# Optimization experiments

Measured on AMD Instinct MI355X. Metric: run time of the kernel, lower is better.

Reference implementation:

```python
import jax, jax.numpy as jnp
import numpy as np

B, S, H = 2, 2048, 2048
N_HEADS = 16
HEAD_DIM = H // N_HEADS  # 128


def apply_rotary(x, cos, sin):
    # x: (B, n_heads, S, head_dim); cos/sin: (S, head_dim//2)
    d = x.shape[-1] // 2
    x1, x2 = x[..., :d], x[..., d:]
    c = cos[None, None, :x.shape[2]]
    s = sin[None, None, :x.shape[2]]
    return jnp.concatenate([x1 * c - x2 * s, x2 * c + x1 * s], axis=-1)


def setup_inputs() -> dict:
    key = jax.random.key(0)
    k1, k2, k3 = jax.random.split(key, 3)
    x = jax.random.normal(k1, (B, S, H), dtype=jnp.float32)
    qkv_w = jax.random.normal(k2, (3 * H, H), dtype=jnp.float32) * (1.0 / np.sqrt(H))
    o_w = jax.random.normal(k3, (H, H), dtype=jnp.float32) * (1.0 / np.sqrt(H))
    # rotary tables, half head_dim
    inv_freq = 1.0 / (10000.0 ** (jnp.arange(0, HEAD_DIM // 2, dtype=jnp.float32) / (HEAD_DIM // 2)))
    t = jnp.arange(S, dtype=jnp.float32)
    freqs = jnp.outer(t, inv_freq)  # (S, head_dim//2)
    cos, sin = jnp.cos(freqs), jnp.sin(freqs)
    # True = masked (strictly upper triangular)
    causal_mask = jnp.triu(jnp.ones((S, S), dtype=bool), k=1)
    return {"x": x, "qkv_w": qkv_w, "o_w": o_w, "cos": cos, "sin": sin,
            "causal_mask": causal_mask}


def reference(x, qkv_w, o_w, cos, sin, causal_mask):
    Bx, Sx, Hx = x.shape
    qkv = jnp.einsum('bsh,oh->bso', x, qkv_w)  # (B,S,3H)
    qkv = qkv.reshape(Bx, Sx, 3, N_HEADS, HEAD_DIM)
    q, k, v = qkv[:, :, 0], qkv[:, :, 1], qkv[:, :, 2]
    q = jnp.transpose(q, (0, 2, 1, 3))  # (B,nh,S,hd)
    k = jnp.transpose(k, (0, 2, 1, 3))
    v = jnp.transpose(v, (0, 2, 1, 3))
    q = apply_rotary(q, cos, sin)
    k = apply_rotary(k, cos, sin)
    scale = 1.0 / jnp.sqrt(jnp.asarray(HEAD_DIM, dtype=x.dtype))
    attn = jnp.einsum('bnqd,bnkd->bnqk', q, k) * scale
    attn = jnp.where(causal_mask[None, None], -jnp.inf, attn)
    attn = jax.nn.softmax(attn, axis=-1)
    out = jnp.einsum('bnqk,bnkd->bnqd', attn, v)
    out = jnp.transpose(out, (0, 2, 1, 3)).reshape(Bx, Sx, Hx)
    return jnp.einsum('bsh,oh->bso', out, o_w)
```

## Files before the change

### kernel.cpp

```cpp
#include <hip/hip_runtime.h>
#include <hip/hip_bf16.h>
#include <stdint.h>

typedef __attribute__((ext_vector_type(4))) float f32x4;
typedef __attribute__((ext_vector_type(8))) short s16x8;
typedef __attribute__((ext_vector_type(4))) short s16x4;

#define SWZ(g, row) ((((g) & ~7) | (((g) ^ ((row) & 7)) & 7)))

__device__ __forceinline__ unsigned short f2bf(float f) {
  unsigned u = __builtin_bit_cast(unsigned, f);
  u += 0x7fffu + ((u >> 16) & 1u);
  return (unsigned short)(u >> 16);
}

__device__ __forceinline__ void gld16(const void* g, void* l) {
  __builtin_amdgcn_global_load_lds(
      (const __attribute__((address_space(1))) void*)g,
      (__attribute__((address_space(3))) void*)l, 16, 0, 0);
}

__global__ void cvt_f32_to_bf16(const float* __restrict__ src,
                                unsigned short* __restrict__ dst, int n4) {
  int i = blockIdx.x * blockDim.x + threadIdx.x;
  if (i >= n4) return;
  float4 v = ((const float4*)src)[i];
  s16x4 o;
  o[0] = (short)f2bf(v.x); o[1] = (short)f2bf(v.y);
  o[2] = (short)f2bf(v.z); o[3] = (short)f2bf(v.w);
  ((s16x4*)dst)[i] = o;
}

template<int EPI>
__global__ __launch_bounds__(256) void gemm_bt(
    const unsigned short* __restrict__ A,
    const unsigned short* __restrict__ Bt,
    float* __restrict__ C, int N, int K,
    const float* __restrict__ cosT, const float* __restrict__ sinT,
    unsigned short* __restrict__ qOut, unsigned short* __restrict__ kOut,
    unsigned short* __restrict__ vtOut)
{
  __shared__ char smem[32768];
  const int tid = (int)threadIdx.x;
  const int w  = tid >> 6, l = tid & 63;
  const int lg = l & 15, hg = l >> 4;
  const int bn0 = (int)blockIdx.x * 128, bm0 = (int)blockIdx.y * 128;

  f32x4 acc[2][8] = {};
  const int nkt = K >> 6;
  for (int kt = 0; kt < nkt; ++kt) {
    __syncthreads();
    for (int i = 0; i < 4; ++i) {
      const int G = w * 256 + i * 64 + l;
      const int row = G >> 3, g = G & 7;
      const int gs = SWZ(g, row);
      gld16((const char*)(A  + (size_t)(bm0 + row) * K + (size_t)kt * 64) + (gs << 4),
            smem + w * 4096 + i * 1024);
      gld16((const char*)(Bt + (size_t)(bn0 + row) * K + (size_t)kt * 64) + (gs << 4),
            smem + 16384 + w * 4096 + i * 1024);
    }
    asm volatile("s_waitcnt vmcnt(0)" ::: "memory");
    __syncthreads();
    for (int ks = 0; ks < 2; ++ks) {
      s16x8 af[2], bfr[8];
      for (int ai = 0; ai < 2; ++ai) {
        const int ra = w * 32 + ai * 16 + lg;
        const int gr = SWZ(4 * ks + hg, ra);
        af[ai] = *(const s16x8*)(smem + ra * 128 + (gr << 4));
      }
      for (int bi = 0; bi < 8; ++bi) {
        const int rb = bi * 16 + lg;
        const int gr = SWZ(4 * ks + hg, rb);
        bfr[bi] = *(const s16x8*)(smem + 16384 + rb * 128 + (gr << 4));
      }
      for (int ai = 0; ai < 2; ++ai)
        for (int bi = 0; bi < 8; ++bi)
          acc[ai][bi] = __builtin_amdgcn_mfma_f32_16x16x32_bf16(
              af[ai], bfr[bi], acc[ai][bi], 0, 0, 0);
    }
  }

  if constexpr (EPI == 0) {
    for (int ai = 0; ai < 2; ++ai)
      for (int bi = 0; bi < 8; ++bi) {
        const int col  = bn0 + bi * 16 + lg;
        const int row0 = bm0 + w * 32 + ai * 16 + hg * 4;
        for (int r = 0; r < 4; ++r)
          C[(size_t)(row0 + r) * N + col] = acc[ai][bi][r];
      }
  } else {
    const int t = bn0 >> 11;
    const int h = (bn0 >> 7) & 15;
    if (t < 2) {
      unsigned short* dst = (t == 0) ? qOut : kOut;
      for (int ai = 0; ai < 2; ++ai)
        for (int bi = 0; bi < 4; ++bi)
          for (int r = 0; r < 4; ++r) {
            const int gr = bm0 + w * 32 + ai * 16 + hg * 4 + r;
            const int b = gr >> 11, s1 = gr & 2047;
            const int c0 = bi * 16 + lg;
            const float x1 = acc[ai][bi][r];
            const float x2 = acc[ai][bi + 4][r];
            const float cv = cosT[s1 * 64 + c0];
            const float sv = sinT[s1 * 64 + c0];
            const size_t base = ((((size_t)b * 16 + h) * 2048) + s1) * 128;
            dst[base + c0]      = f2bf(x1 * cv - x2 * sv);
            dst[base + c0 + 64] = f2bf(x2 * cv + x1 * sv);
          }
    } else {
      for (int ai = 0; ai < 2; ++ai)
        for (int bi = 0; bi < 8; ++bi) {
          const int gr0 = bm0 + w * 32 + ai * 16 + hg * 4;
          const int b = gr0 >> 11, s0 = gr0 & 2047;
          const int d = bi * 16 + lg;
          s16x4 pk;
          for (int r = 0; r < 4; ++r) pk[r] = (short)f2bf(acc[ai][bi][r]);
          *(s16x4*)(vtOut + ((((size_t)b * 16 + h) * 128) + d) * 2048 + s0) = pk;
        }
    }
  }
}

__global__ __launch_bounds__(256) void attn_fwd(
    const unsigned short* __restrict__ Qp, const unsigned short* __restrict__ Kp,
    const unsigned short* __restrict__ Vt, unsigned short* __restrict__ AO)
{
  __shared__ char sK[16384];
  __shared__ char sV[16384];
  __shared__ char sP[8192];

  const int tid = (int)threadIdx.x, w = tid >> 6, l = tid & 63;
  const int lg = l & 15, hg = l >> 4;
  const int bid = (int)blockIdx.x;
  const int p = bid >> 8, c = bid & 255;
  const int j = c >> 5, bh = c & 31;
  const int qt = (p == 0) ? j : (p == 1) ? 31 - j : (p == 2) ? 8 + j : 23 - j;
  const size_t qkBase = (size_t)bh * 2048 * 128;
  const int qw0 = qt * 64 + w * 16;
  const int qi = qw0 + lg;

  s16x8 qf[4];
  for (int ks = 0; ks < 4; ++ks)
    qf[ks] = *(const s16x8*)(Qp + qkBase + (size_t)(qw0 + lg) * 128 + ks * 32 + hg * 8);

  f32x4 acc_o[8] = {};
  float mrun = -1e30f, lrun = 0.f;
  const float SCALE = 0.08838834764831845f;
  const float L2E = 1.4426950408889634f;
  const float CS = SCALE * L2E;

  const int nkv = qt + 1;
  for (int kv = 0; kv < nkv; ++kv) {
    const int kv0 = kv * 64;
    __syncthreads();
    for (int i = 0; i < 4; ++i) {
      const int G = w * 256 + i * 64 + l;
      const int rk = G >> 4, gk = G & 15;
      gld16((const char*)(Kp + qkBase + (size_t)(kv0 + rk) * 128) + (SWZ(gk, rk) << 4),
            sK + w * 4096 + i * 1024);
      const int rv = G >> 3, gv = G & 7;
      gld16((const char*)(Vt + qkBase + (size_t)rv * 2048 + kv0) + (SWZ(gv, rv) << 4),
            sV + w * 4096 + i * 1024);
    }
    asm volatile("s_waitcnt vmcnt(0)" ::: "memory");
    __syncthreads();

    f32x4 accs[4] = {};
    for (int ks = 0; ks < 4; ++ks)
      for (int kf = 0; kf < 4; ++kf) {
        const int row = kf * 16 + lg;
        const int g = SWZ(4 * ks + hg, row);
        s16x8 kfrag = *(const s16x8*)(sK + row * 256 + (g << 4));
        accs[kf] = __builtin_amdgcn_mfma_f32_16x16x32_bf16(kfrag, qf[ks], accs[kf], 0, 0, 0);
      }

    const bool diag = (kv == qt);
    float raw[4][4];
    float mt = -1e30f;
    #pragma unroll
    for (int kf = 0; kf < 4; ++kf)
      #pragma unroll
      for (int r = 0; r < 4; ++r) {
        float s = accs[kf][r];
        if (diag) {
          const int jj = kv0 + kf * 16 + hg * 4 + r;
          s = (jj > qi) ? -1e30f : s;
        }
        raw[kf][r] = s;
        mt = fmaxf(mt, s);
      }
    mt = fmaxf(mt, __shfl_xor(mt, 16));
    mt = fmaxf(mt, __shfl_xor(mt, 32));
    mt *= SCALE;
    if (!__all(mt - mrun <= 8.0f)) {
      const float mnew = fmaxf(mrun, mt);
      const float alpha = exp2f((mrun - mnew) * L2E);
      float ar[4];
      #pragma unroll
      for (int r = 0; r < 4; ++r) ar[r] = __shfl(alpha, hg * 4 + r);
      #pragma unroll
      for (int f = 0; f < 8; ++f)
        #pragma unroll
        for (int r = 0; r < 4; ++r) acc_o[f][r] *= ar[r];
      lrun *= alpha;
      mrun = mnew;
    }
    const float mL = mrun * L2E;
    float ls = 0.f;
    char* pw = sP + w * 2048;
    #pragma unroll
    for (int kf = 0; kf < 4; ++kf) {
      s16x4 pk;
      #pragma unroll
      for (int r = 0; r < 4; ++r) {
        const float e = exp2f(raw[kf][r] * CS - mL);
        ls += e;
        pk[r] = (short)f2bf(e);
      }
      const int j0 = kf * 16 + hg * 4;
      *(s16x4*)(pw + lg * 128 + (SWZ(j0 >> 3, lg) << 4) + ((j0 * 2) & 15)) = pk;
    }
    ls += __shfl_xor(ls, 16);
    ls += __shfl_xor(ls, 32);
    lrun += ls;
    asm volatile("" ::: "memory");

    for (int jc = 0; jc < 2; ++jc) {
      const int gp = SWZ(hg + 4 * jc, lg);
      s16x8 pa = *(const s16x8*)(pw + lg * 128 + (gp << 4));
      for (int f = 0; f < 8; ++f) {
        const int rv = f * 16 + lg;
        const int gv = SWZ(hg + 4 * jc, rv);
        s16x8 vb = *(const s16x8*)(sV + rv * 128 + (gv << 4));
        acc_o[f] = __builtin_amdgcn_mfma_f32_16x16x32_bf16(pa, vb, acc_o[f], 0, 0, 0);
      }
    }
  }

  float linv[4];
  for (int r = 0; r < 4; ++r) linv[r] = 1.0f / __shfl(lrun, hg * 4 + r);
  const int b = bh >> 4, h = bh & 15;
  for (int f = 0; f < 8; ++f) {
    const int d = h * 128 + f * 16 + lg;
    for (int r = 0; r < 4; ++r) {
      const int srow = qw0 + hg * 4 + r;
      AO[((size_t)(b * 2048 + srow)) * 2048 + d] = f2bf(acc_o[f][r] * linv[r]);
    }
  }
}

extern "C" void kernel_launch(void* const* d_in, const int* in_sizes, int n_in,
                              void* d_out, int out_size, void* d_ws, size_t ws_size,
                              hipStream_t stream) {
  const float* x    = (const float*)d_in[0];
  const float* qkvw = (const float*)d_in[1];
  const float* ow   = (const float*)d_in[2];
  const float* cosT = (const float*)d_in[3];
  const float* sinT = (const float*)d_in[4];
  float* out = (float*)d_out;

  unsigned short* X16  = (unsigned short*)d_ws;
  unsigned short* W16  = X16  + (size_t)8388608;
  unsigned short* OW16 = W16  + (size_t)12582912;
  unsigned short* Qp   = OW16 + (size_t)4194304;
  unsigned short* Kp   = Qp   + (size_t)8388608;
  unsigned short* Vtp  = Kp   + (size_t)8388608;
  unsigned short* AO   = Vtp  + (size_t)8388608;

  cvt_f32_to_bf16<<<8192, 256, 0, stream>>>(x, X16, 2097152);
  cvt_f32_to_bf16<<<12288, 256, 0, stream>>>(qkvw, W16, 3145728);
  cvt_f32_to_bf16<<<4096, 256, 0, stream>>>(ow, OW16, 1048576);

  dim3 g1(48, 32);
  gemm_bt<1><<<g1, 256, 0, stream>>>(X16, W16, nullptr, 6144, 2048,
                                     cosT, sinT, Qp, Kp, Vtp);

  attn_fwd<<<1024, 256, 0, stream>>>(Qp, Kp, Vtp, AO);

  dim3 g2(16, 32);
  gemm_bt<0><<<g2, 256, 0, stream>>>(AO, OW16, out, 2048, 2048,
                                     nullptr, nullptr, nullptr, nullptr, nullptr);
}
```

Measured before the change: 266.3 us.

## Replace QKV GEMM with 256x256 double-buffered 8-wave pipelined kernel

Adds a dedicated QKV projection kernel that uses 256x256 output tiles, 512 threads, and 128KB of double-buffered LDS. Global-to-LDS loads for the next K-tile are interleaved with MFMA phases, using explicit waitcnt, barriers and setprio, and blocks are remapped across XCDs. The aim is more data reuse per tile and latency hiding compared with the old 128x128 single-buffered GEMM. The cost is one block per CU and a schedule that is hard-coded for K=2048 and these exact shapes.

```diff
diff --git a/kernel.cpp b/kernel.cpp
--- a/kernel.cpp
+++ b/kernel.cpp
@@ -31,14 +31,126 @@
   ((s16x4*)dst)[i] = o;
 }
 
+#define STG(ORG, LDSB, HALF, KT) \
+  gld16((const char*)((ORG) + ((size_t)((HALF)*128 + srow)) * 2048 + (size_t)(KT) * 64) + gsw, (LDSB) + (HALF) * 16384 + wid * 2048); \
+  gld16((const char*)((ORG) + ((size_t)((HALF)*128 + srow + 8)) * 2048 + (size_t)(KT) * 64) + gsw, (LDSB) + (HALF) * 16384 + wid * 2048 + 1024);
+
+#define PH(MQ, NQ, ENDWAIT, ...) \
+  { s16x8 af[4][2], bv[2][2]; \
+    _Pragma("unroll") for (int j = 0; j < 4; ++j) { \
+      const int ra = (MQ)*128 + wm*64 + j*16 + lg; \
+      _Pragma("unroll") for (int ks = 0; ks < 2; ++ks) \
+        af[j][ks] = *(const s16x8*)(sAc + ra*128 + (((ks*4+hg)^(ra&7)) << 4)); } \
+    _Pragma("unroll") for (int j2 = 0; j2 < 2; ++j2) { \
+      const int rb = (NQ)*128 + wn*16 + j2*64 + lg; \
+      _Pragma("unroll") for (int ks = 0; ks < 2; ++ks) \
+        bv[j2][ks] = *(const s16x8*)(sBc + rb*128 + (((ks*4+hg)^(rb&7)) << 4)); } \
+    __VA_ARGS__ \
+    __builtin_amdgcn_s_barrier(); \
+    asm volatile("s_waitcnt lgkmcnt(0)" ::: "memory"); \
+    __builtin_amdgcn_sched_barrier(0); \
+    __builtin_amdgcn_s_setprio(1); \
+    _Pragma("unroll") for (int j = 0; j < 4; ++j) \
+      _Pragma("unroll") for (int j2 = 0; j2 < 2; ++j2) \
+        _Pragma("unroll") for (int ks = 0; ks < 2; ++ks) \
+          acc[(MQ)*4+j][(NQ)*2+j2] = __builtin_amdgcn_mfma_f32_16x16x32_bf16( \
+              af[j][ks], bv[j2][ks], acc[(MQ)*4+j][(NQ)*2+j2], 0, 0, 0); \
+    __builtin_amdgcn_s_setprio(0); \
+    ENDWAIT \
+    __builtin_amdgcn_s_barrier(); }
+
+__global__ __launch_bounds__(512, 1) void gemm_qkv_256(
+    const unsigned short* __restrict__ A,
+    const unsigned short* __restrict__ Bt,
+    const float* __restrict__ cosT, const float* __restrict__ sinT,
+    unsigned short* __restrict__ qOut, unsigned short* __restrict__ kOut,
+    unsigned short* __restrict__ vtOut)
+{
+  __shared__ char smem[131072];
+  const int tid = (int)threadIdx.x;
+  const int wid = tid >> 6, l = tid & 63;
+  const int lg = l & 15, hg = l >> 4;
+  const int wm = wid >> 2, wn = wid & 3;
+  const int s = ((int)blockIdx.x & 7) * 48 + ((int)blockIdx.x >> 3);
+  const int bm0 = (s & 15) * 256, bn0 = (s >> 4) * 256;
+
+  const int srow = wid * 16 + (l >> 3);
+  const int gsw = ((l & 7) ^ (l >> 3)) << 4;
+
+  const unsigned short* Aorg = A + (size_t)bm0 * 2048;
+  const unsigned short* Borg = Bt + (size_t)bn0 * 2048;
+
+  f32x4 acc[8][4] = {};
+
+  STG(Aorg, smem + 0, 0, 0)
+  STG(Borg, smem + 32768, 0, 0)
+  STG(Borg, smem + 32768, 1, 0)
+  STG(Aorg, smem + 0, 1, 0)
+  asm volatile("s_waitcnt vmcnt(4)" ::: "memory");
+  __builtin_amdgcn_s_barrier();
+
+  for (int t = 0; t < 31; ++t) {
+    const char* sAc = smem + (t & 1) * 65536;
+    const char* sBc = sAc + 32768;
+    char* dA = smem + (((t & 1) ^ 1) * 65536);
+    char* dB = dA + 32768;
+    PH(0, 0, asm volatile("s_waitcnt vmcnt(4)" ::: "memory");, STG(Aorg, dA, 0, t + 1))
+    PH(0, 1, asm volatile("s_waitcnt vmcnt(4)" ::: "memory");, STG(Borg, dB, 0, t + 1))
+    PH(1, 0, , STG(Borg, dB, 1, t + 1))
+    PH(1, 1, asm volatile("s_waitcnt vmcnt(4)" ::: "memory");, STG(Aorg, dA, 1, t + 1))
+  }
+  {
+    const char* sAc = smem + 65536;
+    const char* sBc = sAc + 32768;
+    PH(0, 0, asm volatile("s_waitcnt vmcnt(2)" ::: "memory");, )
+    PH(0, 1, asm volatile("s_waitcnt vmcnt(0)" ::: "memory");, )
+    PH(1, 0, , )
+    PH(1, 1, , )
+  }
+
+  #pragma unroll
+  for (int a = 0; a < 8; ++a) {
+    const int gr0 = bm0 + (a >> 2) * 128 + wm * 64 + (a & 3) * 16 + hg * 4;
+    #pragma unroll
+    for (int pb = 0; pb < 2; ++pb) {
+      const int obase = bn0 + pb * 128;
+      const int tt = obase >> 11;
+      const int h = (obase >> 7) & 15;
+      const int d = wn * 16 + lg;
+      if (tt < 2) {
+        unsigned short* dst = (tt == 0) ? qOut : kOut;
+        #pragma unroll
+        for (int r = 0; r < 4; ++r) {
+          const int gr = gr0 + r;
+          const int b = gr >> 11, s1 = gr & 2047;
+          const float x1 = acc[a][pb * 2 + 0][r];
+          const float x2 = acc[a][pb * 2 + 1][r];
+          const float cv = cosT[s1 * 64 + d];
+          const float sv = sinT[s1 * 64 + d];
+          const size_t base = (((size_t)b * 16 + h) * 2048 + s1) * 128;
+          dst[base + d]      = f2bf(x1 * cv - x2 * sv);
+          dst[base + d + 64] = f2bf(x2 * cv + x1 * sv);
+        }
+      } else {
+        const int b = gr0 >> 11, s0 = gr0 & 2047;
+        s16x4 p1, p2;
+        #pragma unroll
+        for (int r = 0; r < 4; ++r) {
+          p1[r] = (short)f2bf(acc[a][pb * 2 + 0][r]);
+          p2[r] = (short)f2bf(acc[a][pb * 2 + 1][r]);
+        }
+        *(s16x4*)(vtOut + (((size_t)b * 16 + h) * 128 + d)      * 2048 + s0) = p1;
+        *(s16x4*)(vtOut + (((size_t)b * 16 + h) * 128 + d + 64) * 2048 + s0) = p2;
+      }
+    }
+  }
+}
+
 template<int EPI>
 __global__ __launch_bounds__(256) void gemm_bt(
     const unsigned short* __restrict__ A,
     const unsigned short* __restrict__ Bt,
-    float* __restrict__ C, int N, int K,
-    const float* __restrict__ cosT, const float* __restrict__ sinT,
-    unsigned short* __restrict__ qOut, unsigned short* __restrict__ kOut,
-    unsigned short* __restrict__ vtOut)
+    float* __restrict__ C, int N, int K)
 {
   __shared__ char smem[32768];
   const int tid = (int)threadIdx.x;
@@ -80,45 +192,13 @@
     }
   }
 
-  if constexpr (EPI == 0) {
-    for (int ai = 0; ai < 2; ++ai)
-      for (int bi = 0; bi < 8; ++bi) {
-        const int col  = bn0 + bi * 16 + lg;
-        const int row0 = bm0 + w * 32 + ai * 16 + hg * 4;
-        for (int r = 0; r < 4; ++r)
-          C[(size_t)(row0 + r) * N + col] = acc[ai][bi][r];
-      }
-  } else {
-    const int t = bn0 >> 11;
-    const int h = (bn0 >> 7) & 15;
-    if (t < 2) {
-      unsigned short* dst = (t == 0) ? qOut : kOut;
-      for (int ai = 0; ai < 2; ++ai)
-        for (int bi = 0; bi < 4; ++bi)
-          for (int r = 0; r < 4; ++r) {
-            const int gr = bm0 + w * 32 + ai * 16 + hg * 4 + r;
-            const int b = gr >> 11, s1 = gr & 2047;
-            const int c0 = bi * 16 + lg;
-            const float x1 = acc[ai][bi][r];
-            const float x2 = acc[ai][bi + 4][r];
-            const float cv = cosT[s1 * 64 + c0];
-            const float sv = sinT[s1 * 64 + c0];
-            const size_t base = ((((size_t)b * 16 + h) * 2048) + s1) * 128;
-            dst[base + c0]      = f2bf(x1 * cv - x2 * sv);
-            dst[base + c0 + 64] = f2bf(x2 * cv + x1 * sv);
-          }
-    } else {
-      for (int ai = 0; ai < 2; ++ai)
-        for (int bi = 0; bi < 8; ++bi) {
-          const int gr0 = bm0 + w * 32 + ai * 16 + hg * 4;
-          const int b = gr0 >> 11, s0 = gr0 & 2047;
-          const int d = bi * 16 + lg;
-          s16x4 pk;
-          for (int r = 0; r < 4; ++r) pk[r] = (short)f2bf(acc[ai][bi][r]);
-          *(s16x4*)(vtOut + ((((size_t)b * 16 + h) * 128) + d) * 2048 + s0) = pk;
-        }
-    }
-  }
+  for (int ai = 0; ai < 2; ++ai)
+    for (int bi = 0; bi < 8; ++bi) {
+      const int col  = bn0 + bi * 16 + lg;
+      const int row0 = bm0 + w * 32 + ai * 16 + hg * 4;
+      for (int r = 0; r < 4; ++r)
+        C[(size_t)(row0 + r) * N + col] = acc[ai][bi][r];
+    }
 }
 
 __global__ __launch_bounds__(256) void attn_fwd(
@@ -271,13 +351,10 @@
   cvt_f32_to_bf16<<<12288, 256, 0, stream>>>(qkvw, W16, 3145728);
   cvt_f32_to_bf16<<<4096, 256, 0, stream>>>(ow, OW16, 1048576);
 
-  dim3 g1(48, 32);
-  gemm_bt<1><<<g1, 256, 0, stream>>>(X16, W16, nullptr, 6144, 2048,
-                                     cosT, sinT, Qp, Kp, Vtp);
+  gemm_qkv_256<<<384, 512, 0, stream>>>(X16, W16, cosT, sinT, Qp, Kp, Vtp);
 
   attn_fwd<<<1024, 256, 0, stream>>>(Qp, Kp, Vtp, AO);
 
   dim3 g2(16, 32);
-  gemm_bt<0><<<g2, 256, 0, stream>>>(AO, OW16, out, 2048, 2048,
-                                     nullptr, nullptr, nullptr, nullptr, nullptr);
-}
+  gemm_bt<0><<<g2, 256, 0, stream>>>(AO, OW16, out, 2048, 2048);
+}
```

After: 277.6 us. +4.2%, slower.
